# Performance work log

Hardware: AMD Instinct MI355X
Metric: run time of the kernel (lower is better)

The kernel has to match this reference:

```python
import jax, jax.numpy as jnp
import numpy as np
from jax import lax

WINDOW = 512
HOP = 128
SR = 16000
ALPHA = 1e-06
F = WINDOW // 2 + 1  # 257 bins
GAIN = float(np.sqrt(8.0 / 3.0))

# frequency-domain constants (match PsychoacousticMasker properties)
_freqs = np.linspace(0.0, SR / 2.0, F)
_bark_np = 13.0 * np.arctan(0.00076 * _freqs) + 3.5 * np.arctan((_freqs / 7500.0) ** 2)
_valid_dom = (_freqs >= 20.0) & (_freqs <= 20000.0)
_ath_np = np.full(F, -np.inf)
_fk = _freqs[_valid_dom] * 0.001
_ath_np[_valid_dom] = 3.64 * _fk ** -0.8 - 6.5 * np.exp(-0.6 * (_fk - 3.3) ** 2) + 0.001 * _fk ** 4 - 12.0
BARK = jnp.asarray(_bark_np, jnp.float32)
ATH = jnp.asarray(_ath_np, jnp.float32)
DELTA_SHIFT = -6.025 - 0.275 * BARK
HANN = jnp.asarray(0.5 * (1.0 - np.cos(2.0 * np.pi * np.arange(WINDOW) / WINDOW)), jnp.float32)


def _stft(x):
    # center=False hann STFT -> [n_frames, F] complex
    n_frames = (x.shape[0] - WINDOW) // HOP + 1
    idx = jnp.arange(n_frames)[:, None] * HOP + jnp.arange(WINDOW)[None, :]
    return jnp.fft.rfft(x[idx] * HANN, axis=-1)


def _frame_threshold(p):
    # p: [F] SPL-normalized PSD (dB) for one frame -> global masking threshold [F]
    interior = (p[1:-1] > p[:-2]) & (p[1:-1] > p[2:])
    is_max = jnp.pad(interior, (1, 1), constant_values=False)
    pw = 10.0 ** (p / 10.0)
    m_all = 10.0 * jnp.log10(pw + jnp.roll(pw, 1) + jnp.roll(pw, -1))  # tonal masker level (bins j-1,j,j+1)
    valid = is_max & (m_all > ATH)
    order = jnp.argsort((~valid).astype(jnp.int32))  # stable: valid bins first, in frequency order
    vmask = valid[order]
    m_c = jnp.where(vmask, m_all[order], -200.0)     # compacted masker dB values
    n = valid.sum()

    def step(carry, i):
        i_prev, keep = carry
        active = i < n
        # NB: source indexes bark[] with masker *list positions* (i, i_prev); replicated faithfully
        close = (BARK[i] - BARK[i_prev]) < 0.5
        prev_smaller = m_c[i_prev] < m_c[i]
        del_idx = jnp.where(prev_smaller, i_prev, i)
        keep = jnp.where(active & close, keep.at[del_idx].set(False), keep)
        i_prev = jnp.where(active, jnp.where(close, jnp.where(prev_smaller, i_prev + 1, i_prev), i), i_prev)
        return (i_prev, keep), None

    (_, keep), _ = lax.scan(step, (jnp.int32(0), jnp.ones(F, dtype=bool)), jnp.arange(1, F, dtype=jnp.int32))
    keep = keep & vmask
    # individual thresholds, vectorized over maskers k and bins
    z_j = BARK[order]                                    # bark of each masker's bin
    dz = BARK[None, :] - z_j[:, None]                    # [K, F]
    slope = jnp.where(dz > 0, -27.0 + 0.37 * jnp.maximum(m_c - 40.0, 0.0)[:, None], 27.0)
    t = m_c[:, None] + DELTA_SHIFT[order][:, None] + slope * dz
    power = jnp.where(keep[:, None], 10.0 ** (t / 10.0), 0.0)
    return 10.0 * jnp.log10(power.sum(0) + 10.0 ** (ATH / 10.0))


def _threshold_and_psd_max(audio):
    s = _stft(audio)                                     # [T, F]
    psd = 20.0 * jnp.log10(jnp.abs(GAIN * s / WINDOW))
    psd = jnp.maximum(psd, -200.0)
    psd_max = psd.max()
    psd_n = 96.0 - psd_max + psd
    thr = jax.vmap(_frame_threshold)(psd_n)              # [T, F]
    return thr, psd_max


def setup_inputs() -> dict:
    key = jax.random.key(0)
    k1, k2 = jax.random.split(key)
    L = 160000  # 10 s @ 16 kHz; (L - 512) % 128 == 0 -> 1247 frames, pad is a no-op
    x_ref = 0.5 * jax.random.normal(k1, (L,), dtype=jnp.float32)
    x_adv = x_ref + 0.01 * jax.random.normal(k2, (L,), dtype=jnp.float32)
    return {"x_adv": x_adv, "x_ref": x_ref}


def reference(x_adv, x_ref):
    thr, psd_max = _threshold_and_psd_max(x_ref)
    thr = lax.stop_gradient(thr)
    psd_max = lax.stop_gradient(psd_max)
    delta = x_adv - x_ref
    sd = _stft(delta)                                    # [T, F]
    psd_d = (GAIN / WINDOW) ** 2 * (sd.real ** 2 + sd.imag ** 2)
    psd_d = (10.0 ** 9.6) / (10.0 ** (psd_max / 10.0)) * psd_d
    loss = jnp.mean(jax.nn.relu(psd_d - 10.0 ** (thr / 10.0)))
    return ALPHA * loss
```

## Files before the change

kernel.cpp:

```cpp
#include <hip/hip_runtime.h>
#include <math.h>


#define FBINS 257

#define TAB_BARK  0
#define TAB_ATHDB 257
#define TAB_ATHP  514
#define TAB_HANN  771
#define TAB_TWR   1283
#define TAB_TWI   1539
#define TAB_FLOATS 2048

__global__ __launch_bounds__(256) void k0_init(float* __restrict__ tab)
{
    const int tid = threadIdx.x;
    const double TWO_PI = 6.283185307179586476925286766559;
    for (int f = tid; f < FBINS; f += 256) {
        double freq = 31.25 * (double)f;
        double q    = freq / 7500.0;
        tab[TAB_BARK + f] = (float)(13.0 * atan(0.00076 * freq) + 3.5 * atan(q * q));
        if (f == 0) {
            tab[TAB_ATHDB] = -INFINITY;
            tab[TAB_ATHP]  = 0.0f;
        } else {
            double fk = freq * 0.001;
            double ad = 3.64 * pow(fk, -0.8)
                      - 6.5 * exp(-0.6 * (fk - 3.3) * (fk - 3.3))
                      + 0.001 * fk * fk * fk * fk - 12.0;
            float av = (float)ad;
            tab[TAB_ATHDB + f] = av;
            tab[TAB_ATHP  + f] = exp10f(av / 10.0f);
        }
    }
    for (int n = tid; n < 512; n += 256) {
        double cw = cos((TWO_PI * (double)n) / 512.0);
        tab[TAB_HANN + n] = (float)(0.5 * (1.0 - cw));
    }
    for (int j = tid; j < 256; j += 256) {
        double s, c;
        sincos(-(TWO_PI / 512.0) * (double)j, &s, &c);
        tab[TAB_TWR + j] = (float)c;
        tab[TAB_TWI + j] = (float)s;
    }
}

__global__ __launch_bounds__(256) void k1_stft(
    const float* __restrict__ xadv, const float* __restrict__ xref,
    const float* __restrict__ tab,
    float* __restrict__ psd_db, float* __restrict__ pd, float* __restrict__ fmaxs)
{
    __shared__ float re[512], im[512], twr[256], twi[256];
    __shared__ float wmax[4];
    const int t = blockIdx.x, tid = threadIdx.x;

    twr[tid] = tab[TAB_TWR + tid];
    twi[tid] = tab[TAB_TWI + tid];

    const int base_idx = t * 128;
    for (int n = tid; n < 512; n += 256) {
        float w = tab[TAB_HANN + n];
        float r = xref[base_idx + n];
        float a = xadv[base_idx + n];
        int   p = __brev((unsigned)n) >> 23;
        re[p] = w * r;
        im[p] = w * (a - r);
    }
    __syncthreads();

    for (int stage = 1; stage <= 9; ++stage) {
        int half  = 1 << (stage - 1);
        int tstep = 512 >> stage;
        int j     = tid & (half - 1);
        int base  = ((tid >> (stage - 1)) << stage) + j;
        float wr = twr[j * tstep], wi = twi[j * tstep];
        float vr0 = re[base + half], vi0 = im[base + half];
        float vr = vr0 * wr - vi0 * wi;
        float vi = vr0 * wi + vi0 * wr;
        float ur = re[base], ui = im[base];
        __syncthreads();
        re[base]        = ur + vr; im[base]        = ui + vi;
        re[base + half] = ur - vr; im[base + half] = ui - vi;
        __syncthreads();
    }

    const float S2 = 1.0172526041666667e-05f;
    float lmax = -1e30f;
    for (int k = tid; k <= 256; k += 256) {
        int nk = (512 - k) & 511;
        float zr = re[k],  zi = im[k];
        float yr = re[nk], yi = im[nk];
        float ar = 0.5f * (zr + yr), ai = 0.5f * (zi - yi);
        float br = 0.5f * (zi + yi), bi = 0.5f * (yr - zr);
        float prefp = S2 * (ar * ar + ai * ai);
        float pdb   = fmaxf(10.0f * log10f(prefp), -200.0f);
        psd_db[t * FBINS + k] = pdb;
        pd[t * FBINS + k]     = S2 * (br * br + bi * bi);
        lmax = fmaxf(lmax, pdb);
    }
    for (int off = 32; off > 0; off >>= 1) lmax = fmaxf(lmax, __shfl_down(lmax, off));
    if ((tid & 63) == 0) wmax[tid >> 6] = lmax;
    __syncthreads();
    if (tid == 0)
        fmaxs[t] = fmaxf(fmaxf(wmax[0], wmax[1]), fmaxf(wmax[2], wmax[3]));
}

__global__ __launch_bounds__(256) void k2_max(
    const float* __restrict__ fmaxs, int nf, float* __restrict__ psdmax)
{
    __shared__ float sm[4];
    float v = -1e30f;
    for (int i = threadIdx.x; i < nf; i += 256) v = fmaxf(v, fmaxs[i]);
    for (int off = 32; off > 0; off >>= 1) v = fmaxf(v, __shfl_down(v, off));
    if ((threadIdx.x & 63) == 0) sm[threadIdx.x >> 6] = v;
    __syncthreads();
    if (threadIdx.x == 0)
        psdmax[0] = fmaxf(fmaxf(sm[0], sm[1]), fmaxf(sm[2], sm[3]));
}

__global__ __launch_bounds__(256) void k3_threshold(
    const float* __restrict__ tab,
    const float* __restrict__ psd_db, const float* __restrict__ pd,
    const float* __restrict__ psdmax, float* __restrict__ floss)
{
    __shared__ float barkf[FBINS], athp_s[FBINS];
    __shared__ float p_s[FBINS], pw_s[FBINS];
    __shared__ float mc_s[128], shift_s[128], barkm_s[128], ups_s[128];
    __shared__ int   bin_s[128], keep_s[128];
    __shared__ int   wcnt[4];
    __shared__ float red[4];

    const int t = blockIdx.x, tid = threadIdx.x;
    const int lane = tid & 63, wid = tid >> 6;
    const float pmax   = psdmax[0];
    const float shift0 = 96.0f - pmax;

    for (int f = tid; f < FBINS; f += 256) {
        barkf[f]  = tab[TAB_BARK + f];
        athp_s[f] = tab[TAB_ATHP + f];
        float pv = shift0 + psd_db[t * FBINS + f];
        p_s[f]  = pv;
        pw_s[f] = exp10f(pv / 10.0f);
    }
    __syncthreads();

    float m = -1e30f;
    int   pred = 0;
    if (tid >= 1 && tid <= 255) {
        float pc = p_s[tid];
        if (pc > p_s[tid - 1] && pc > p_s[tid + 1]) {
            m = 10.0f * log10f((pw_s[tid] + pw_s[tid - 1]) + pw_s[tid + 1]);
            if (m > tab[TAB_ATHDB + tid]) pred = 1;
        }
    }
    unsigned long long bal = __ballot(pred);
    if (lane == 0) wcnt[wid] = __popcll(bal);
    __syncthreads();
    int base = 0;
    for (int w = 0; w < wid; ++w) base += wcnt[w];
    const int n_total = wcnt[0] + wcnt[1] + wcnt[2] + wcnt[3];
    if (pred) {
        int pos = base + __popcll(bal & ((1ull << lane) - 1));
        bin_s[pos] = tid; mc_s[pos] = m; keep_s[pos] = 1;
    }
    __syncthreads();

    if (tid == 0) {
        int i_prev = 0;
        for (int i = 1; i < n_total; ++i) {
            bool close        = (barkf[i] - barkf[i_prev]) < 0.5f;
            bool prev_smaller = mc_s[i_prev] < mc_s[i];
            if (close) {
                keep_s[prev_smaller ? i_prev : i] = 0;
                if (prev_smaller) i_prev = i_prev + 1;
            } else {
                i_prev = i;
            }
        }
    }
    __syncthreads();

    int pred2 = (tid < n_total) && keep_s[tid];
    unsigned long long bal2 = __ballot(pred2);
    if (lane == 0) wcnt[wid] = __popcll(bal2);
    __syncthreads();
    int base2 = 0;
    for (int w = 0; w < wid; ++w) base2 += wcnt[w];
    const int nk = wcnt[0] + wcnt[1] + wcnt[2] + wcnt[3];
    if (pred2) {
        int pos = base2 + __popcll(bal2 & ((1ull << lane) - 1));
        int   fb = bin_s[tid];
        float mc = mc_s[tid];
        shift_s[pos] = mc + (-6.025f - 0.275f * barkf[fb]);
        barkm_s[pos] = barkf[fb];
        ups_s[pos]   = -27.0f + 0.37f * fmaxf(mc - 40.0f, 0.0f);
    }
    __syncthreads();

    const float C = 3981071705.534973f / exp10f(pmax / 10.0f);
    float lsum = 0.0f;
    for (int f = tid; f < FBINS; f += 256) {
        float bf  = barkf[f];
        float acc = 0.0f;
        for (int k = 0; k < nk; ++k) {
            float dz    = bf - barkm_s[k];
            float slope = (dz > 0.0f) ? ups_s[k] : 27.0f;
            float tdb   = shift_s[k] + slope * dz;
            acc += exp10f(tdb / 10.0f);
        }
        float thrpow = acc + athp_s[f];
        float pds    = C * pd[t * FBINS + f];
        lsum += fmaxf(pds - thrpow, 0.0f);
    }
    for (int off = 32; off > 0; off >>= 1) lsum += __shfl_down(lsum, off);
    if ((tid & 63) == 0) red[tid >> 6] = lsum;
    __syncthreads();
    if (tid == 0) floss[t] = (red[0] + red[1]) + (red[2] + red[3]);
}

__global__ __launch_bounds__(256) void k4_final(
    const float* __restrict__ floss, int nf, float* __restrict__ out)
{
    __shared__ float red[4];
    float s = 0.0f;
    for (int i = threadIdx.x; i < nf; i += 256) s += floss[i];
    for (int off = 32; off > 0; off >>= 1) s += __shfl_down(s, off);
    if ((threadIdx.x & 63) == 0) red[threadIdx.x >> 6] = s;
    __syncthreads();
    if (threadIdx.x == 0) {
        float total = (red[0] + red[1]) + (red[2] + red[3]);
        out[0] = 1e-6f * (total / (float)(nf * FBINS));
    }
}

extern "C" void kernel_launch(void* const* d_in, const int* in_sizes, int n_in,
                              void* d_out, int out_size, void* d_ws, size_t ws_size,
                              hipStream_t stream)
{
    const float* x_adv = (const float*)d_in[0];
    const float* x_ref = (const float*)d_in[1];
    float*       out   = (float*)d_out;

    const int L  = in_sizes[0];
    const int nf = (L - 512) / 128 + 1;

    float* ws      = (float*)d_ws;
    float* tab     = ws;
    float* psd_db  = ws + TAB_FLOATS;
    float* pd      = psd_db + (size_t)nf * FBINS;
    float* fmaxs   = pd + (size_t)nf * FBINS;
    float* floss   = fmaxs + nf;
    float* psdmax  = floss + nf;

    k0_init     <<<1,  256, 0, stream>>>(tab);
    k1_stft     <<<nf, 256, 0, stream>>>(x_adv, x_ref, tab, psd_db, pd, fmaxs);
    k2_max      <<<1,  256, 0, stream>>>(fmaxs, nf, psdmax);
    k3_threshold<<<nf, 256, 0, stream>>>(tab, psd_db, pd, psdmax, floss);
    k4_final    <<<1,  256, 0, stream>>>(floss, nf, out);
}
```

Measured before the change: 93.29 us.

## Fold max and final reductions into threshold kernel, ping-pong padded float2 FFT

```diff
diff --git a/kernel.cpp b/kernel.cpp
--- a/kernel.cpp
+++ b/kernel.cpp
@@ -12,36 +12,44 @@
 #define TAB_TWI   1539
 #define TAB_FLOATS 2048
 
-__global__ __launch_bounds__(256) void k0_init(float* __restrict__ tab)
+__device__ __forceinline__ int swz(int i) { return i + (i >> 4); }
+
+__global__ __launch_bounds__(256) void k0_init(
+    float* __restrict__ tab, float* __restrict__ acc, unsigned int* __restrict__ ticket)
 {
     const int tid = threadIdx.x;
     const double TWO_PI = 6.283185307179586476925286766559;
-    for (int f = tid; f < FBINS; f += 256) {
-        double freq = 31.25 * (double)f;
-        double q    = freq / 7500.0;
-        tab[TAB_BARK + f] = (float)(13.0 * atan(0.00076 * freq) + 3.5 * atan(q * q));
-        if (f == 0) {
-            tab[TAB_ATHDB] = -INFINITY;
-            tab[TAB_ATHP]  = 0.0f;
-        } else {
-            double fk = freq * 0.001;
-            double ad = 3.64 * pow(fk, -0.8)
-                      - 6.5 * exp(-0.6 * (fk - 3.3) * (fk - 3.3))
-                      + 0.001 * fk * fk * fk * fk - 12.0;
-            float av = (float)ad;
-            tab[TAB_ATHDB + f] = av;
-            tab[TAB_ATHP  + f] = exp10f(av / 10.0f);
-        }
-    }
-    for (int n = tid; n < 512; n += 256) {
-        double cw = cos((TWO_PI * (double)n) / 512.0);
-        tab[TAB_HANN + n] = (float)(0.5 * (1.0 - cw));
-    }
-    for (int j = tid; j < 256; j += 256) {
-        double s, c;
-        sincos(-(TWO_PI / 512.0) * (double)j, &s, &c);
-        tab[TAB_TWR + j] = (float)c;
-        tab[TAB_TWI + j] = (float)s;
+    if (blockIdx.x == 0) {
+        if (tid == 0) { acc[0] = 0.0f; ticket[0] = 0u; }
+        for (int f = tid; f < FBINS; f += 256) {
+            double freq = 31.25 * (double)f;
+            double q    = freq / 7500.0;
+            tab[TAB_BARK + f] = (float)(13.0 * atan(0.00076 * freq) + 3.5 * atan(q * q));
+            if (f == 0) {
+                tab[TAB_ATHDB] = -INFINITY;
+                tab[TAB_ATHP]  = 0.0f;
+            } else {
+                double fk = freq * 0.001;
+                double ad = 3.64 * pow(fk, -0.8)
+                          - 6.5 * exp(-0.6 * (fk - 3.3) * (fk - 3.3))
+                          + 0.001 * fk * fk * fk * fk - 12.0;
+                float av = (float)ad;
+                tab[TAB_ATHDB + f] = av;
+                tab[TAB_ATHP  + f] = exp10f(av / 10.0f);
+            }
+        }
+    } else if (blockIdx.x == 1) {
+        for (int n = tid; n < 512; n += 256) {
+            double cw = cos((TWO_PI * (double)n) / 512.0);
+            tab[TAB_HANN + n] = (float)(0.5 * (1.0 - cw));
+        }
+    } else {
+        for (int j = tid; j < 256; j += 256) {
+            double s, c;
+            sincos(-(TWO_PI / 512.0) * (double)j, &s, &c);
+            tab[TAB_TWR + j] = (float)c;
+            tab[TAB_TWI + j] = (float)s;
+        }
     }
 }
 
@@ -50,12 +58,12 @@
     const float* __restrict__ tab,
     float* __restrict__ psd_db, float* __restrict__ pd, float* __restrict__ fmaxs)
 {
-    __shared__ float re[512], im[512], twr[256], twi[256];
+    __shared__ float2 z[2][544];
+    __shared__ float2 tw[272];
     __shared__ float wmax[4];
     const int t = blockIdx.x, tid = threadIdx.x;
 
-    twr[tid] = tab[TAB_TWR + tid];
-    twi[tid] = tab[TAB_TWI + tid];
+    tw[swz(tid)] = make_float2(tab[TAB_TWR + tid], tab[TAB_TWI + tid]);
 
     const int base_idx = t * 128;
     for (int n = tid; n < 512; n += 256) {
@@ -63,24 +71,24 @@
         float r = xref[base_idx + n];
         float a = xadv[base_idx + n];
         int   p = __brev((unsigned)n) >> 23;
-        re[p] = w * r;
-        im[p] = w * (a - r);
-    }
-    __syncthreads();
-
+        z[0][swz(p)] = make_float2(w * r, w * (a - r));
+    }
+    __syncthreads();
+
+    int cur = 0;
     for (int stage = 1; stage <= 9; ++stage) {
         int half  = 1 << (stage - 1);
         int tstep = 512 >> stage;
         int j     = tid & (half - 1);
         int base  = ((tid >> (stage - 1)) << stage) + j;
-        float wr = twr[j * tstep], wi = twi[j * tstep];
-        float vr0 = re[base + half], vi0 = im[base + half];
-        float vr = vr0 * wr - vi0 * wi;
-        float vi = vr0 * wi + vi0 * wr;
-        float ur = re[base], ui = im[base];
-        __syncthreads();
-        re[base]        = ur + vr; im[base]        = ui + vi;
-        re[base + half] = ur - vr; im[base + half] = ui - vi;
+        float2 w  = tw[swz(j * tstep)];
+        float2 u  = z[cur][swz(base)];
+        float2 v  = z[cur][swz(base + half)];
+        float vr = v.x * w.x - v.y * w.y;
+        float vi = v.x * w.y + v.y * w.x;
+        z[cur ^ 1][swz(base)]        = make_float2(u.x + vr, u.y + vi);
+        z[cur ^ 1][swz(base + half)] = make_float2(u.x - vr, u.y - vi);
+        cur ^= 1;
         __syncthreads();
     }
 
@@ -88,10 +96,10 @@
     float lmax = -1e30f;
     for (int k = tid; k <= 256; k += 256) {
         int nk = (512 - k) & 511;
-        float zr = re[k],  zi = im[k];
-        float yr = re[nk], yi = im[nk];
-        float ar = 0.5f * (zr + yr), ai = 0.5f * (zi - yi);
-        float br = 0.5f * (zi + yi), bi = 0.5f * (yr - zr);
+        float2 zk = z[cur][swz(k)];
+        float2 zn = z[cur][swz(nk)];
+        float ar = 0.5f * (zk.x + zn.x), ai = 0.5f * (zk.y - zn.y);
+        float br = 0.5f * (zk.y + zn.y), bi = 0.5f * (zn.x - zk.x);
         float prefp = S2 * (ar * ar + ai * ai);
         float pdb   = fmaxf(10.0f * log10f(prefp), -200.0f);
         psd_db[t * FBINS + k] = pdb;
@@ -105,23 +113,12 @@
         fmaxs[t] = fmaxf(fmaxf(wmax[0], wmax[1]), fmaxf(wmax[2], wmax[3]));
 }
 
-__global__ __launch_bounds__(256) void k2_max(
-    const float* __restrict__ fmaxs, int nf, float* __restrict__ psdmax)
-{
-    __shared__ float sm[4];
-    float v = -1e30f;
-    for (int i = threadIdx.x; i < nf; i += 256) v = fmaxf(v, fmaxs[i]);
-    for (int off = 32; off > 0; off >>= 1) v = fmaxf(v, __shfl_down(v, off));
-    if ((threadIdx.x & 63) == 0) sm[threadIdx.x >> 6] = v;
-    __syncthreads();
-    if (threadIdx.x == 0)
-        psdmax[0] = fmaxf(fmaxf(sm[0], sm[1]), fmaxf(sm[2], sm[3]));
-}
-
 __global__ __launch_bounds__(256) void k3_threshold(
     const float* __restrict__ tab,
     const float* __restrict__ psd_db, const float* __restrict__ pd,
-    const float* __restrict__ psdmax, float* __restrict__ floss)
+    const float* __restrict__ fmaxs, int nf,
+    float* __restrict__ acc, unsigned int* __restrict__ ticket,
+    float* __restrict__ out)
 {
     __shared__ float barkf[FBINS], athp_s[FBINS];
     __shared__ float p_s[FBINS], pw_s[FBINS];
@@ -129,15 +126,24 @@
     __shared__ int   bin_s[128], keep_s[128];
     __shared__ int   wcnt[4];
     __shared__ float red[4];
+    __shared__ float smax[4];
 
     const int t = blockIdx.x, tid = threadIdx.x;
     const int lane = tid & 63, wid = tid >> 6;
-    const float pmax   = psdmax[0];
-    const float shift0 = 96.0f - pmax;
 
     for (int f = tid; f < FBINS; f += 256) {
         barkf[f]  = tab[TAB_BARK + f];
         athp_s[f] = tab[TAB_ATHP + f];
+    }
+    float v = -1e30f;
+    for (int i = tid; i < nf; i += 256) v = fmaxf(v, fmaxs[i]);
+    for (int off = 32; off > 0; off >>= 1) v = fmaxf(v, __shfl_down(v, off));
+    if (lane == 0) smax[wid] = v;
+    __syncthreads();
+    const float pmax   = fmaxf(fmaxf(smax[0], smax[1]), fmaxf(smax[2], smax[3]));
+    const float shift0 = 96.0f - pmax;
+
+    for (int f = tid; f < FBINS; f += 256) {
         float pv = shift0 + psd_db[t * FBINS + f];
         p_s[f]  = pv;
         pw_s[f] = exp10f(pv / 10.0f);
@@ -201,35 +207,30 @@
     float lsum = 0.0f;
     for (int f = tid; f < FBINS; f += 256) {
         float bf  = barkf[f];
-        float acc = 0.0f;
+        float acc2 = 0.0f;
         for (int k = 0; k < nk; ++k) {
             float dz    = bf - barkm_s[k];
             float slope = (dz > 0.0f) ? ups_s[k] : 27.0f;
             float tdb   = shift_s[k] + slope * dz;
-            acc += exp10f(tdb / 10.0f);
-        }
-        float thrpow = acc + athp_s[f];
+            acc2 += exp10f(tdb / 10.0f);
+        }
+        float thrpow = acc2 + athp_s[f];
         float pds    = C * pd[t * FBINS + f];
         lsum += fmaxf(pds - thrpow, 0.0f);
     }
     for (int off = 32; off > 0; off >>= 1) lsum += __shfl_down(lsum, off);
     if ((tid & 63) == 0) red[tid >> 6] = lsum;
     __syncthreads();
-    if (tid == 0) floss[t] = (red[0] + red[1]) + (red[2] + red[3]);
-}
-
-__global__ __launch_bounds__(256) void k4_final(
-    const float* __restrict__ floss, int nf, float* __restrict__ out)
-{
-    __shared__ float red[4];
-    float s = 0.0f;
-    for (int i = threadIdx.x; i < nf; i += 256) s += floss[i];
-    for (int off = 32; off > 0; off >>= 1) s += __shfl_down(s, off);
-    if ((threadIdx.x & 63) == 0) red[threadIdx.x >> 6] = s;
-    __syncthreads();
-    if (threadIdx.x == 0) {
+
+    if (tid == 0) {
         float total = (red[0] + red[1]) + (red[2] + red[3]);
-        out[0] = 1e-6f * (total / (float)(nf * FBINS));
+        atomicAdd(acc, total);
+        __threadfence();
+        unsigned int old = atomicAdd(ticket, 1u);
+        if (old == (unsigned int)(nf - 1)) {
+            float tot = atomicAdd(acc, 0.0f);
+            out[0] = 1e-6f * (tot / (float)(nf * FBINS));
+        }
     }
 }
 
@@ -249,12 +250,10 @@
     float* psd_db  = ws + TAB_FLOATS;
     float* pd      = psd_db + (size_t)nf * FBINS;
     float* fmaxs   = pd + (size_t)nf * FBINS;
-    float* floss   = fmaxs + nf;
-    float* psdmax  = floss + nf;
-
-    k0_init     <<<1,  256, 0, stream>>>(tab);
+    float* acc     = fmaxs + nf;
+    unsigned int* ticket = (unsigned int*)(acc + 1);
+
+    k0_init     <<<3,  256, 0, stream>>>(tab, acc, ticket);
     k1_stft     <<<nf, 256, 0, stream>>>(x_adv, x_ref, tab, psd_db, pd, fmaxs);
-    k2_max      <<<1,  256, 0, stream>>>(fmaxs, nf, psdmax);
-    k3_threshold<<<nf, 256, 0, stream>>>(tab, psd_db, pd, psdmax, floss);
-    k4_final    <<<1,  256, 0, stream>>>(floss, nf, out);
-}
+    k3_threshold<<<nf, 256, 0, stream>>>(tab, psd_db, pd, fmaxs, nf, acc, ticket, out);
+}
```

Result: slower. 111.6 us (+19.7%).
